# Performance work log

Measured on AMD Instinct MI355X. Metric: run time of the kernel, lower is better.

## Reference

```python
import jax, jax.numpy as jnp
import numpy as np

B, D, H = 16384, 1024, 16
HD = D // H
EPS = 1e-5


def setup_inputs() -> dict:
    key = jax.random.key(0)
    ks = jax.random.split(key, 16)
    w = lambda k, shape: jax.random.normal(k, shape, jnp.float32) * 0.02
    return {
        "img_emb": jax.random.normal(ks[0], (B, D), jnp.float32),
        "txt_emb": jax.random.normal(ks[1], (B, D), jnp.float32),
        "route_choice": jax.random.randint(ks[2], (B,), 0, 3, jnp.int32),
        # gate: Linear(2D -> D) + sigmoid
        "Wg": w(ks[3], (2 * D, D)), "bg": jnp.zeros((D,), jnp.float32),
        # MultiheadAttention in/out projections
        "Wqkv": w(ks[4], (D, 3 * D)), "bqkv": jnp.zeros((3 * D,), jnp.float32),
        "Wo": w(ks[5], (D, D)), "bo": jnp.zeros((D,), jnp.float32),
        # LayerNorm
        "gamma": jnp.ones((D,), jnp.float32), "beta": jnp.zeros((D,), jnp.float32),
        # FFN: Linear(D->4D), GELU, Linear(4D->D)
        "Wf1": w(ks[6], (D, 4 * D)), "bf1": jnp.zeros((4 * D,), jnp.float32),
        "Wf2": w(ks[7], (4 * D, D)), "bf2": jnp.zeros((D,), jnp.float32),
    }


def _layernorm(x, gamma, beta):
    mu = jnp.mean(x, axis=-1, keepdims=True)
    var = jnp.mean(jnp.square(x - mu), axis=-1, keepdims=True)
    return (x - mu) * jax.lax.rsqrt(var + EPS) * gamma + beta


def reference(img_emb, txt_emb, route_choice, Wg, bg, Wqkv, bqkv, Wo, bo,
              gamma, beta, Wf1, bf1, Wf2, bf2):
    # Eval mode: energy_loss = 0, no dropout. Routing choice supplied as int input.
    # Compute the 'full' fusion branch densely, then select per sample.
    ri = jnp.concatenate([img_emb, txt_emb], axis=-1)          # [B, 2D]
    gate = jax.nn.sigmoid(ri @ Wg + bg)                        # [B, D]
    fused = gate * img_emb + (1.0 - gate) * txt_emb            # [B, D]

    x = jnp.stack([img_emb, txt_emb], axis=1)                  # [B, 2, D]
    qkv = x @ Wqkv + bqkv                                      # [B, 2, 3D]
    q, k, v = jnp.split(qkv, 3, axis=-1)
    q = q.reshape(B, 2, H, HD)
    k = k.reshape(B, 2, H, HD)
    v = v.reshape(B, 2, H, HD)
    scores = jnp.einsum("bqhd,bkhd->bhqk", q, k) / np.sqrt(HD) # [B, H, 2, 2]
    attn = jax.nn.softmax(scores, axis=-1)
    ctx = jnp.einsum("bhqk,bkhd->bqhd", attn, v).reshape(B, 2, D)
    attn_out = ctx @ Wo + bo                                   # [B, 2, D]

    fused = fused + attn_out.mean(axis=1)
    fused = _layernorm(fused, gamma, beta)
    full_out = jax.nn.gelu(fused @ Wf1 + bf1, approximate=False) @ Wf2 + bf2

    rc = route_choice[:, None]
    out = jnp.where(rc == 0, img_emb, jnp.where(rc == 1, txt_emb, full_out))
    return out
```

## Files before the change

### kernel.cpp

```cpp
#include <hip/hip_runtime.h>
#include <hip/hip_bf16.h>
#include <math.h>

#define NB 16384
#define DIM 1024
#define CAP 6656

using bf16 = __hip_bfloat16;
typedef __attribute__((ext_vector_type(8))) short short8;
typedef __attribute__((ext_vector_type(4))) short short4v;
typedef __attribute__((ext_vector_type(4))) float float4v;

enum { EPI_QKV = 1, EPI_GELU = 3, EPI_OUT = 4 };

__device__ __forceinline__ void gl_lds16(const void* g, void* l) {
  __builtin_amdgcn_global_load_lds(
      (const __attribute__((address_space(1))) unsigned int*)g,
      (__attribute__((address_space(3))) unsigned int*)l, 16, 0, 0);
}

__device__ __forceinline__ short f2bf(float x) {
  __hip_bfloat16 h = __float2bfloat16(x);
  return *reinterpret_cast<short*>(&h);
}

__global__ __launch_bounds__(256) void transpose_cast(
    const float* __restrict__ in, bf16* __restrict__ out, int K, int N) {
  __shared__ float tile[32][33];
  int n0 = blockIdx.x * 32, k0 = blockIdx.y * 32;
  int tx = threadIdx.x, ty = threadIdx.y;
#pragma unroll
  for (int i = 0; i < 32; i += 8)
    tile[ty + i][tx] = in[(size_t)(k0 + ty + i) * N + n0 + tx];
  __syncthreads();
#pragma unroll
  for (int i = 0; i < 32; i += 8)
    out[(size_t)(n0 + ty + i) * K + k0 + tx] = __float2bfloat16(tile[tx][ty + i]);
}

__global__ void zero_cnt(int* cnt) { if (threadIdx.x == 0) *cnt = 0; }

__global__ __launch_bounds__(256) void index_build(const int* __restrict__ route,
                                                   int* __restrict__ cnt,
                                                   int* __restrict__ idx) {
  int r = blockIdx.x * 256 + threadIdx.x;
  if (r < NB && route[r] == 2) {
    int p = atomicAdd(cnt, 1);
    idx[p] = r;
  }
}

__global__ __launch_bounds__(256) void gather_cast(
    const float* __restrict__ img, const float* __restrict__ txt,
    const int* __restrict__ cnt, const int* __restrict__ idx,
    bf16* __restrict__ xg, bf16* __restrict__ tg) {
  int n = blockIdx.x;
  if (n >= *cnt) return;
  int r = idx[n];
  int c = threadIdx.x * 4;
  float4 vi = *(const float4*)(img + (size_t)r * DIM + c);
  float4 vt = *(const float4*)(txt + (size_t)r * DIM + c);
  short4v pi, pt;
  pi[0] = f2bf(vi.x); pi[1] = f2bf(vi.y); pi[2] = f2bf(vi.z); pi[3] = f2bf(vi.w);
  pt[0] = f2bf(vt.x); pt[1] = f2bf(vt.y); pt[2] = f2bf(vt.z); pt[3] = f2bf(vt.w);
  *(short4v*)(xg + (size_t)n * DIM + c) = pi;
  *(short4v*)(tg + (size_t)n * DIM + c) = pt;
}

template <int EPI>
__global__ __launch_bounds__(256) void gemm_k(
    const bf16* __restrict__ A0, const bf16* __restrict__ Bt,
    const float* __restrict__ bias, void* __restrict__ outp, int ldo,
    const int* __restrict__ cntp, const int* __restrict__ idx, int K) {
  const int cnt = *cntp;
  const int m0 = blockIdx.y * 128;
  if (m0 >= ((cnt + 127) & ~127)) return;
  alignas(16) __shared__ bf16 sA[128 * 32];
  alignas(16) __shared__ bf16 sB[128 * 32];
  const int t = threadIdx.x;
  const int wave = t >> 6, lane = t & 63;
  const int wm = (wave >> 1) * 64, wn = (wave & 1) * 64;
  const int n0 = blockIdx.x * 128;
  const int r16 = lane & 15, quad = lane >> 4;

  float4v acc[4][4] = {};

  for (int k0 = 0; k0 < K; k0 += 32) {
    if (k0) __syncthreads();
#pragma unroll
    for (int j = 0; j < 2; ++j) {
      int c = t + j * 256;
      int row = c >> 2;
      int kk = k0 + (c & 3) * 8;
      gl_lds16(Bt + (size_t)(n0 + row) * K + kk, (void*)(sB + j * 2048 + wave * 512));
      gl_lds16(A0 + (size_t)(m0 + row) * K + kk, (void*)(sA + j * 2048 + wave * 512));
    }
    __syncthreads();
    short8 af[4], bfr[4];
#pragma unroll
    for (int i = 0; i < 4; ++i) {
      af[i] = *(const short8*)(sA + (wm + i * 16 + r16) * 32 + quad * 8);
      bfr[i] = *(const short8*)(sB + (wn + i * 16 + r16) * 32 + quad * 8);
    }
#pragma unroll
    for (int i = 0; i < 4; ++i)
#pragma unroll
      for (int j = 0; j < 4; ++j)
        acc[i][j] =
            __builtin_amdgcn_mfma_f32_16x16x32_bf16(af[i], bfr[j], acc[i][j], 0, 0, 0);
  }

#pragma unroll
  for (int i = 0; i < 4; ++i) {
#pragma unroll
    for (int j = 0; j < 4; ++j) {
      int gcol = n0 + wn + j * 16 + r16;
      float bv = bias[gcol];
#pragma unroll
      for (int r = 0; r < 4; ++r) {
        int grow = m0 + wm + i * 16 + quad * 4 + r;
        float v = acc[i][j][r] + bv;
        if constexpr (EPI == EPI_QKV) {
          ((bf16*)outp)[(size_t)grow * ldo + gcol] = __float2bfloat16(v);
        } else if constexpr (EPI == EPI_GELU) {
          float gl = 0.5f * v * (1.f + erff(v * 0.70710678118654752f));
          ((bf16*)outp)[(size_t)grow * ldo + gcol] = __float2bfloat16(gl);
        } else {
          if (grow < cnt) {
            int orow = idx[grow];
            ((float*)outp)[(size_t)orow * DIM + gcol] = v;
          }
        }
      }
    }
  }
}

__global__ __launch_bounds__(256) void gate_z_kernel(
    const float* __restrict__ img, const float* __restrict__ txt,
    const bf16* __restrict__ xg, const bf16* __restrict__ tg,
    const bf16* __restrict__ WgT, const float* __restrict__ bg,
    const bf16* __restrict__ WoT, const float* __restrict__ bo,
    const bf16* __restrict__ cmean, bf16* __restrict__ z,
    const int* __restrict__ cntp, const int* __restrict__ idx) {
  const int cnt = *cntp;
  const int m0 = blockIdx.y * 128;
  if (m0 >= ((cnt + 127) & ~127)) return;
  alignas(16) __shared__ bf16 sA[128 * 32];
  alignas(16) __shared__ bf16 sB[128 * 32];
  const int t = threadIdx.x;
  const int wave = t >> 6, lane = t & 63;
  const int wm = (wave >> 1) * 64, wn = (wave & 1) * 64;
  const int n0 = blockIdx.x * 128;
  const int r16 = lane & 15, quad = lane >> 4;

  float4v acc[4][4] = {};
  for (int k0 = 0; k0 < 2048; k0 += 32) {
    if (k0) __syncthreads();
#pragma unroll
    for (int j = 0; j < 2; ++j) {
      int c = t + j * 256;
      int row = c >> 2;
      int kk = k0 + (c & 3) * 8;
      gl_lds16(WgT + (size_t)(n0 + row) * 2048 + kk, (void*)(sB + j * 2048 + wave * 512));
      const bf16* ga = (kk < DIM) ? xg + (size_t)(m0 + row) * DIM + kk
                                  : tg + (size_t)(m0 + row) * DIM + (kk - DIM);
      gl_lds16(ga, (void*)(sA + j * 2048 + wave * 512));
    }
    __syncthreads();
    short8 af[4], bfr[4];
#pragma unroll
    for (int i = 0; i < 4; ++i) {
      af[i] = *(const short8*)(sA + (wm + i * 16 + r16) * 32 + quad * 8);
      bfr[i] = *(const short8*)(sB + (wn + i * 16 + r16) * 32 + quad * 8);
    }
#pragma unroll
    for (int i = 0; i < 4; ++i)
#pragma unroll
      for (int j = 0; j < 4; ++j)
        acc[i][j] =
            __builtin_amdgcn_mfma_f32_16x16x32_bf16(af[i], bfr[j], acc[i][j], 0, 0, 0);
  }
  float4v fmix[4][4];
#pragma unroll
  for (int i = 0; i < 4; ++i)
#pragma unroll
    for (int j = 0; j < 4; ++j) {
      int gcol = n0 + wn + j * 16 + r16;
      float bv = bg[gcol];
#pragma unroll
      for (int r = 0; r < 4; ++r) {
        int grow = m0 + wm + i * 16 + quad * 4 + r;
        float fm = 0.f;
        if (grow < cnt) {
          int orow = idx[grow];
          float g = 1.f / (1.f + expf(-(acc[i][j][r] + bv)));
          size_t ii = (size_t)orow * DIM + gcol;
          fm = g * img[ii] + (1.f - g) * txt[ii];
        }
        fmix[i][j][r] = fm;
        acc[i][j][r] = 0.f;
      }
    }
  __syncthreads();
  for (int k0 = 0; k0 < 1024; k0 += 32) {
    if (k0) __syncthreads();
#pragma unroll
    for (int j = 0; j < 2; ++j) {
      int c = t + j * 256;
      int row = c >> 2;
      int kk = k0 + (c & 3) * 8;
      gl_lds16(cmean + (size_t)(m0 + row) * 1024 + kk, (void*)(sA + j * 2048 + wave * 512));
      gl_lds16(WoT + (size_t)(n0 + row) * 1024 + kk, (void*)(sB + j * 2048 + wave * 512));
    }
    __syncthreads();
    short8 af[4], bfr[4];
#pragma unroll
    for (int i = 0; i < 4; ++i) {
      af[i] = *(const short8*)(sA + (wm + i * 16 + r16) * 32 + quad * 8);
      bfr[i] = *(const short8*)(sB + (wn + i * 16 + r16) * 32 + quad * 8);
    }
#pragma unroll
    for (int i = 0; i < 4; ++i)
#pragma unroll
      for (int j = 0; j < 4; ++j)
        acc[i][j] =
            __builtin_amdgcn_mfma_f32_16x16x32_bf16(af[i], bfr[j], acc[i][j], 0, 0, 0);
  }
#pragma unroll
  for (int i = 0; i < 4; ++i)
#pragma unroll
    for (int j = 0; j < 4; ++j) {
      int gcol = n0 + wn + j * 16 + r16;
      float bv = bo[gcol];
#pragma unroll
      for (int r = 0; r < 4; ++r) {
        int grow = m0 + wm + i * 16 + quad * 4 + r;
        z[(size_t)grow * DIM + gcol] =
            __float2bfloat16(fmix[i][j][r] + acc[i][j][r] + bv);
      }
    }
}

__global__ __launch_bounds__(256) void attn_kernel(const bf16* __restrict__ qkv,
                                                   bf16* __restrict__ cmean,
                                                   const int* __restrict__ cntp) {
  const int cnt = *cntp;
  int gw = blockIdx.x * 4 + (threadIdx.x >> 6);
  int lane = threadIdx.x & 63;
  int n = gw >> 4, h = gw & 15;
  if (n >= ((cnt + 127) & ~127)) return;
  const bf16* b0 = qkv + (size_t)n * 3072 + h * 64 + lane;
  const bf16* b1 = b0 + (size_t)CAP * 3072;
  float q0 = __bfloat162float(b0[0]);
  float k0 = __bfloat162float(b0[1024]);
  float v0 = __bfloat162float(b0[2048]);
  float q1 = __bfloat162float(b1[0]);
  float k1 = __bfloat162float(b1[1024]);
  float v1 = __bfloat162float(b1[2048]);
  float s00 = q0 * k0, s01 = q0 * k1, s10 = q1 * k0, s11 = q1 * k1;
#pragma unroll
  for (int d = 32; d > 0; d >>= 1) {
    s00 += __shfl_xor(s00, d);
    s01 += __shfl_xor(s01, d);
    s10 += __shfl_xor(s10, d);
    s11 += __shfl_xor(s11, d);
  }
  const float sc = 0.125f;
  s00 *= sc; s01 *= sc; s10 *= sc; s11 *= sc;
  float m0 = fmaxf(s00, s01), m1 = fmaxf(s10, s11);
  float e00 = expf(s00 - m0), e01 = expf(s01 - m0);
  float e10 = expf(s10 - m1), e11 = expf(s11 - m1);
  float i0 = 1.f / (e00 + e01), i1 = 1.f / (e10 + e11);
  float c0 = (e00 * i0) * v0 + (e01 * i0) * v1;
  float c1 = (e10 * i1) * v0 + (e11 * i1) * v1;
  cmean[(size_t)n * DIM + h * 64 + lane] = __float2bfloat16(0.5f * (c0 + c1));
}

__global__ __launch_bounds__(256) void ln_kernel(bf16* __restrict__ z,
                                                 const float* __restrict__ g,
                                                 const float* __restrict__ be,
                                                 const int* __restrict__ cntp) {
  const int cnt = *cntp;
  int b = blockIdx.x, t = threadIdx.x;
  if (b >= ((cnt + 127) & ~127)) return;
  bf16* zr = z + (size_t)b * DIM;
  float v[4];
  float s = 0.f, s2 = 0.f;
#pragma unroll
  for (int i = 0; i < 4; ++i) {
    float x = __bfloat162float(zr[t + 256 * i]);
    v[i] = x; s += x; s2 += x * x;
  }
#pragma unroll
  for (int d = 32; d > 0; d >>= 1) {
    s += __shfl_xor(s, d);
    s2 += __shfl_xor(s2, d);
  }
  __shared__ float rs[4], rs2[4];
  int w = t >> 6, lane = t & 63;
  if (!lane) { rs[w] = s; rs2[w] = s2; }
  __syncthreads();
  s = rs[0] + rs[1] + rs[2] + rs[3];
  s2 = rs2[0] + rs2[1] + rs2[2] + rs2[3];
  float mu = s * (1.f / 1024.f);
  float var = s2 * (1.f / 1024.f) - mu * mu;
  float r = rsqrtf(var + 1e-5f);
#pragma unroll
  for (int i = 0; i < 4; ++i) {
    int c = t + 256 * i;
    zr[c] = __float2bfloat16((v[i] - mu) * r * g[c] + be[c]);
  }
}

__global__ __launch_bounds__(256) void copy_out(const float* __restrict__ img,
                                                const float* __restrict__ txt,
                                                const int* __restrict__ route,
                                                float* __restrict__ out) {
  int row = blockIdx.x;
  int rc = route[row];
  if (rc == 2) return;
  const float* src = rc == 0 ? img : txt;
  int c = threadIdx.x * 4;
  *(float4*)(out + (size_t)row * DIM + c) = *(const float4*)(src + (size_t)row * DIM + c);
}

extern "C" void kernel_launch(void* const* d_in, const int* in_sizes, int n_in,
                              void* d_out, int out_size, void* d_ws, size_t ws_size,
                              hipStream_t stream) {
  const float* img = (const float*)d_in[0];
  const float* txt = (const float*)d_in[1];
  const int* route = (const int*)d_in[2];
  const float* Wg = (const float*)d_in[3];
  const float* bg = (const float*)d_in[4];
  const float* Wqkv = (const float*)d_in[5];
  const float* bqkv = (const float*)d_in[6];
  const float* Wo = (const float*)d_in[7];
  const float* bo = (const float*)d_in[8];
  const float* gamma = (const float*)d_in[9];
  const float* beta = (const float*)d_in[10];
  const float* Wf1 = (const float*)d_in[11];
  const float* bf1 = (const float*)d_in[12];
  const float* Wf2 = (const float*)d_in[13];
  const float* bf2 = (const float*)d_in[14];

  char* ws = (char*)d_ws;
  size_t off = 0;
  auto alloc = [&](size_t bytes) {
    char* p = ws + off;
    off += (bytes + 255) & ~(size_t)255;
    return p;
  };
  int* cntp = (int*)alloc(256);
  int* idx = (int*)alloc((size_t)NB * 4);
  bf16* WgT = (bf16*)alloc((size_t)1024 * 2048 * 2);
  bf16* WqkvT = (bf16*)alloc((size_t)3072 * 1024 * 2);
  bf16* WoT = (bf16*)alloc((size_t)1024 * 1024 * 2);
  bf16* Wf1T = (bf16*)alloc((size_t)4096 * 1024 * 2);
  bf16* Wf2T = (bf16*)alloc((size_t)1024 * 4096 * 2);
  bf16* xg = (bf16*)alloc((size_t)CAP * 1024 * 2);
  bf16* tg = (bf16*)alloc((size_t)CAP * 1024 * 2);
  bf16* qkvs = (bf16*)alloc((size_t)2 * CAP * 3072 * 2);
  bf16* cmean = (bf16*)alloc((size_t)CAP * 1024 * 2);
  bf16* zb = (bf16*)alloc((size_t)CAP * 1024 * 2);
  bf16* hb = qkvs;

  const int MB = CAP / 128;
  dim3 tblk(32, 8);
  transpose_cast<<<dim3(1024 / 32, 2048 / 32), tblk, 0, stream>>>(Wg, WgT, 2048, 1024);
  transpose_cast<<<dim3(3072 / 32, 1024 / 32), tblk, 0, stream>>>(Wqkv, WqkvT, 1024, 3072);
  transpose_cast<<<dim3(1024 / 32, 1024 / 32), tblk, 0, stream>>>(Wo, WoT, 1024, 1024);
  transpose_cast<<<dim3(4096 / 32, 1024 / 32), tblk, 0, stream>>>(Wf1, Wf1T, 1024, 4096);
  transpose_cast<<<dim3(1024 / 32, 4096 / 32), tblk, 0, stream>>>(Wf2, Wf2T, 4096, 1024);

  zero_cnt<<<1, 64, 0, stream>>>(cntp);
  index_build<<<NB / 256, 256, 0, stream>>>(route, cntp, idx);
  gather_cast<<<CAP, 256, 0, stream>>>(img, txt, cntp, idx, xg, tg);

  gemm_k<EPI_QKV><<<dim3(24, MB), 256, 0, stream>>>(
      xg, WqkvT, bqkv, qkvs, 3072, cntp, idx, 1024);
  gemm_k<EPI_QKV><<<dim3(24, MB), 256, 0, stream>>>(
      tg, WqkvT, bqkv, qkvs + (size_t)CAP * 3072, 3072, cntp, idx, 1024);
  attn_kernel<<<CAP * 4, 256, 0, stream>>>(qkvs, cmean, cntp);
  gate_z_kernel<<<dim3(8, MB), 256, 0, stream>>>(img, txt, xg, tg, WgT, bg, WoT, bo,
                                                 cmean, zb, cntp, idx);
  ln_kernel<<<CAP, 256, 0, stream>>>(zb, gamma, beta, cntp);
  gemm_k<EPI_GELU><<<dim3(32, MB), 256, 0, stream>>>(
      zb, Wf1T, bf1, hb, 4096, cntp, idx, 1024);
  gemm_k<EPI_OUT><<<dim3(8, MB), 256, 0, stream>>>(
      hb, Wf2T, bf2, d_out, 1024, cntp, idx, 4096);
  copy_out<<<NB, 256, 0, stream>>>(img, txt, route, (float*)d_out);
}
```

Measured before the change: 643.5 us.

## Fuse gate GEMM into QKV GEMMs, split-K FFN2, swizzle tiles, merged routed output

The gate linear is split into its image and text halves and appended as extra output columns to each QKV GEMM (N=4096). The separate gate GEMM inside the Wo kernel goes away, and Wo's epilogue reads the two partial gate pre-activations instead. The second FFN GEMM is split over K into two fp32 partial buffers, which are summed with the bias in a route_out kernel that also copies the non-routed rows. This replaces the scattered fp32 writes with coalesced row writes. Block ids are swizzled in groups of 8 N-tiles to improve L2 reuse, at the cost of extra partial-buffer traffic and a few more launches.

```diff
diff --git a/kernel.cpp b/kernel.cpp
--- a/kernel.cpp
+++ b/kernel.cpp
@@ -5,14 +5,13 @@
 #define NB 16384
 #define DIM 1024
 #define CAP 6656
+#define MT 52
 
 using bf16 = __hip_bfloat16;
 typedef __attribute__((ext_vector_type(8))) short short8;
 typedef __attribute__((ext_vector_type(4))) short short4v;
 typedef __attribute__((ext_vector_type(4))) float float4v;
 
-enum { EPI_QKV = 1, EPI_GELU = 3, EPI_OUT = 4 };
-
 __device__ __forceinline__ void gl_lds16(const void* g, void* l) {
   __builtin_amdgcn_global_load_lds(
       (const __attribute__((address_space(1))) unsigned int*)g,
@@ -22,6 +21,16 @@
 __device__ __forceinline__ short f2bf(float x) {
   __hip_bfloat16 h = __float2bfloat16(x);
   return *reinterpret_cast<short*>(&h);
+}
+
+__device__ __forceinline__ void swz(int bid, int nN, int& m0, int& n0) {
+  int x = bid & 7;
+  int r = bid >> 3;
+  int nl = nN >> 3;
+  int nLoc = r % nl;
+  int m = r / nl;
+  n0 = (x + 8 * nLoc) * 128;
+  m0 = m * 128;
 }
 
 __global__ __launch_bounds__(256) void transpose_cast(
@@ -38,15 +47,27 @@
     out[(size_t)(n0 + ty + i) * K + k0 + tx] = __float2bfloat16(tile[tx][ty + i]);
 }
 
+__global__ __launch_bounds__(256) void fill_bias(const float* __restrict__ bqkv,
+                                                 const float* __restrict__ bg,
+                                                 float* __restrict__ biasA,
+                                                 float* __restrict__ biasB) {
+  int i = blockIdx.x * 256 + threadIdx.x;
+  float qv = (i < 3072) ? bqkv[i] : 0.f;
+  biasA[i] = qv;
+  biasB[i] = (i < 3072) ? qv : bg[i - 3072];
+}
+
 __global__ void zero_cnt(int* cnt) { if (threadIdx.x == 0) *cnt = 0; }
 
 __global__ __launch_bounds__(256) void index_build(const int* __restrict__ route,
                                                    int* __restrict__ cnt,
-                                                   int* __restrict__ idx) {
+                                                   int* __restrict__ idx,
+                                                   int* __restrict__ pos) {
   int r = blockIdx.x * 256 + threadIdx.x;
   if (r < NB && route[r] == 2) {
     int p = atomicAdd(cnt, 1);
     idx[p] = r;
+    pos[r] = p;
   }
 }
 
@@ -67,33 +88,32 @@
   *(short4v*)(tg + (size_t)n * DIM + c) = pt;
 }
 
-template <int EPI>
-__global__ __launch_bounds__(256) void gemm_k(
-    const bf16* __restrict__ A0, const bf16* __restrict__ Bt,
-    const float* __restrict__ bias, void* __restrict__ outp, int ldo,
-    const int* __restrict__ cntp, const int* __restrict__ idx, int K) {
-  const int cnt = *cntp;
-  const int m0 = blockIdx.y * 128;
+__global__ __launch_bounds__(256) void gemm_qkvg(
+    const bf16* __restrict__ A0, const bf16* __restrict__ BtQ,
+    const bf16* __restrict__ BtG, const float* __restrict__ bias,
+    bf16* __restrict__ outp, const int* __restrict__ cntp) {
+  const int cnt = *cntp;
+  int m0, n0;
+  swz(blockIdx.x, 32, m0, n0);
   if (m0 >= ((cnt + 127) & ~127)) return;
   alignas(16) __shared__ bf16 sA[128 * 32];
   alignas(16) __shared__ bf16 sB[128 * 32];
   const int t = threadIdx.x;
   const int wave = t >> 6, lane = t & 63;
   const int wm = (wave >> 1) * 64, wn = (wave & 1) * 64;
-  const int n0 = blockIdx.x * 128;
   const int r16 = lane & 15, quad = lane >> 4;
+  const bf16* Bt = (n0 < 3072) ? BtQ + (size_t)n0 * 1024 : BtG + (size_t)(n0 - 3072) * 1024;
 
   float4v acc[4][4] = {};
-
-  for (int k0 = 0; k0 < K; k0 += 32) {
+  for (int k0 = 0; k0 < 1024; k0 += 32) {
     if (k0) __syncthreads();
 #pragma unroll
     for (int j = 0; j < 2; ++j) {
       int c = t + j * 256;
       int row = c >> 2;
       int kk = k0 + (c & 3) * 8;
-      gl_lds16(Bt + (size_t)(n0 + row) * K + kk, (void*)(sB + j * 2048 + wave * 512));
-      gl_lds16(A0 + (size_t)(m0 + row) * K + kk, (void*)(sA + j * 2048 + wave * 512));
+      gl_lds16(Bt + (size_t)row * 1024 + kk, (void*)(sB + j * 2048 + wave * 512));
+      gl_lds16(A0 + (size_t)(m0 + row) * 1024 + kk, (void*)(sA + j * 2048 + wave * 512));
     }
     __syncthreads();
     short8 af[4], bfr[4];
@@ -109,9 +129,8 @@
         acc[i][j] =
             __builtin_amdgcn_mfma_f32_16x16x32_bf16(af[i], bfr[j], acc[i][j], 0, 0, 0);
   }
-
-#pragma unroll
-  for (int i = 0; i < 4; ++i) {
+#pragma unroll
+  for (int i = 0; i < 4; ++i)
 #pragma unroll
     for (int j = 0; j < 4; ++j) {
       int gcol = n0 + wn + j * 16 + r16;
@@ -119,130 +138,13 @@
 #pragma unroll
       for (int r = 0; r < 4; ++r) {
         int grow = m0 + wm + i * 16 + quad * 4 + r;
-        float v = acc[i][j][r] + bv;
-        if constexpr (EPI == EPI_QKV) {
-          ((bf16*)outp)[(size_t)grow * ldo + gcol] = __float2bfloat16(v);
-        } else if constexpr (EPI == EPI_GELU) {
-          float gl = 0.5f * v * (1.f + erff(v * 0.70710678118654752f));
-          ((bf16*)outp)[(size_t)grow * ldo + gcol] = __float2bfloat16(gl);
-        } else {
-          if (grow < cnt) {
-            int orow = idx[grow];
-            ((float*)outp)[(size_t)orow * DIM + gcol] = v;
-          }
-        }
+        outp[(size_t)grow * 4096 + gcol] = __float2bfloat16(acc[i][j][r] + bv);
       }
     }
-  }
-}
-
-__global__ __launch_bounds__(256) void gate_z_kernel(
-    const float* __restrict__ img, const float* __restrict__ txt,
-    const bf16* __restrict__ xg, const bf16* __restrict__ tg,
-    const bf16* __restrict__ WgT, const float* __restrict__ bg,
-    const bf16* __restrict__ WoT, const float* __restrict__ bo,
-    const bf16* __restrict__ cmean, bf16* __restrict__ z,
-    const int* __restrict__ cntp, const int* __restrict__ idx) {
-  const int cnt = *cntp;
-  const int m0 = blockIdx.y * 128;
-  if (m0 >= ((cnt + 127) & ~127)) return;
-  alignas(16) __shared__ bf16 sA[128 * 32];
-  alignas(16) __shared__ bf16 sB[128 * 32];
-  const int t = threadIdx.x;
-  const int wave = t >> 6, lane = t & 63;
-  const int wm = (wave >> 1) * 64, wn = (wave & 1) * 64;
-  const int n0 = blockIdx.x * 128;
-  const int r16 = lane & 15, quad = lane >> 4;
-
-  float4v acc[4][4] = {};
-  for (int k0 = 0; k0 < 2048; k0 += 32) {
-    if (k0) __syncthreads();
-#pragma unroll
-    for (int j = 0; j < 2; ++j) {
-      int c = t + j * 256;
-      int row = c >> 2;
-      int kk = k0 + (c & 3) * 8;
-      gl_lds16(WgT + (size_t)(n0 + row) * 2048 + kk, (void*)(sB + j * 2048 + wave * 512));
-      const bf16* ga = (kk < DIM) ? xg + (size_t)(m0 + row) * DIM + kk
-                                  : tg + (size_t)(m0 + row) * DIM + (kk - DIM);
-      gl_lds16(ga, (void*)(sA + j * 2048 + wave * 512));
-    }
-    __syncthreads();
-    short8 af[4], bfr[4];
-#pragma unroll
-    for (int i = 0; i < 4; ++i) {
-      af[i] = *(const short8*)(sA + (wm + i * 16 + r16) * 32 + quad * 8);
-      bfr[i] = *(const short8*)(sB + (wn + i * 16 + r16) * 32 + quad * 8);
-    }
-#pragma unroll
-    for (int i = 0; i < 4; ++i)
-#pragma unroll
-      for (int j = 0; j < 4; ++j)
-        acc[i][j] =
-            __builtin_amdgcn_mfma_f32_16x16x32_bf16(af[i], bfr[j], acc[i][j], 0, 0, 0);
-  }
-  float4v fmix[4][4];
-#pragma unroll
-  for (int i = 0; i < 4; ++i)
-#pragma unroll
-    for (int j = 0; j < 4; ++j) {
-      int gcol = n0 + wn + j * 16 + r16;
-      float bv = bg[gcol];
-#pragma unroll
-      for (int r = 0; r < 4; ++r) {
-        int grow = m0 + wm + i * 16 + quad * 4 + r;
-        float fm = 0.f;
-        if (grow < cnt) {
-          int orow = idx[grow];
-          float g = 1.f / (1.f + expf(-(acc[i][j][r] + bv)));
-          size_t ii = (size_t)orow * DIM + gcol;
-          fm = g * img[ii] + (1.f - g) * txt[ii];
-        }
-        fmix[i][j][r] = fm;
-        acc[i][j][r] = 0.f;
-      }
-    }
-  __syncthreads();
-  for (int k0 = 0; k0 < 1024; k0 += 32) {
-    if (k0) __syncthreads();
-#pragma unroll
-    for (int j = 0; j < 2; ++j) {
-      int c = t + j * 256;
-      int row = c >> 2;
-      int kk = k0 + (c & 3) * 8;
-      gl_lds16(cmean + (size_t)(m0 + row) * 1024 + kk, (void*)(sA + j * 2048 + wave * 512));
-      gl_lds16(WoT + (size_t)(n0 + row) * 1024 + kk, (void*)(sB + j * 2048 + wave * 512));
-    }
-    __syncthreads();
-    short8 af[4], bfr[4];
-#pragma unroll
-    for (int i = 0; i < 4; ++i) {
-      af[i] = *(const short8*)(sA + (wm + i * 16 + r16) * 32 + quad * 8);
-      bfr[i] = *(const short8*)(sB + (wn + i * 16 + r16) * 32 + quad * 8);
-    }
-#pragma unroll
-    for (int i = 0; i < 4; ++i)
-#pragma unroll
-      for (int j = 0; j < 4; ++j)
-        acc[i][j] =
-            __builtin_amdgcn_mfma_f32_16x16x32_bf16(af[i], bfr[j], acc[i][j], 0, 0, 0);
-  }
-#pragma unroll
-  for (int i = 0; i < 4; ++i)
-#pragma unroll
-    for (int j = 0; j < 4; ++j) {
-      int gcol = n0 + wn + j * 16 + r16;
-      float bv = bo[gcol];
-#pragma unroll
-      for (int r = 0; r < 4; ++r) {
-        int grow = m0 + wm + i * 16 + quad * 4 + r;
-        z[(size_t)grow * DIM + gcol] =
-            __float2bfloat16(fmix[i][j][r] + acc[i][j][r] + bv);
-      }
-    }
-}
-
-__global__ __launch_bounds__(256) void attn_kernel(const bf16* __restrict__ qkv,
+}
+
+__global__ __launch_bounds__(256) void attn_kernel(const bf16* __restrict__ qx,
+                                                   const bf16* __restrict__ tx,
                                                    bf16* __restrict__ cmean,
                                                    const int* __restrict__ cntp) {
   const int cnt = *cntp;
@@ -250,8 +152,8 @@
   int lane = threadIdx.x & 63;
   int n = gw >> 4, h = gw & 15;
   if (n >= ((cnt + 127) & ~127)) return;
-  const bf16* b0 = qkv + (size_t)n * 3072 + h * 64 + lane;
-  const bf16* b1 = b0 + (size_t)CAP * 3072;
+  const bf16* b0 = qx + (size_t)n * 4096 + h * 64 + lane;
+  const bf16* b1 = tx + (size_t)n * 4096 + h * 64 + lane;
   float q0 = __bfloat162float(b0[0]);
   float k0 = __bfloat162float(b0[1024]);
   float v0 = __bfloat162float(b0[2048]);
@@ -277,6 +179,72 @@
   cmean[(size_t)n * DIM + h * 64 + lane] = __float2bfloat16(0.5f * (c0 + c1));
 }
 
+__global__ __launch_bounds__(256) void wo_z_kernel(
+    const float* __restrict__ img, const float* __restrict__ txt,
+    const bf16* __restrict__ qx, const bf16* __restrict__ tx,
+    const bf16* __restrict__ WoT, const float* __restrict__ bg,
+    const float* __restrict__ bo, const bf16* __restrict__ cmean,
+    bf16* __restrict__ z, const int* __restrict__ cntp, const int* __restrict__ idx) {
+  const int cnt = *cntp;
+  int m0, n0;
+  swz(blockIdx.x, 8, m0, n0);
+  if (m0 >= ((cnt + 127) & ~127)) return;
+  alignas(16) __shared__ bf16 sA[128 * 32];
+  alignas(16) __shared__ bf16 sB[128 * 32];
+  const int t = threadIdx.x;
+  const int wave = t >> 6, lane = t & 63;
+  const int wm = (wave >> 1) * 64, wn = (wave & 1) * 64;
+  const int r16 = lane & 15, quad = lane >> 4;
+
+  float4v acc[4][4] = {};
+  for (int k0 = 0; k0 < 1024; k0 += 32) {
+    if (k0) __syncthreads();
+#pragma unroll
+    for (int j = 0; j < 2; ++j) {
+      int c = t + j * 256;
+      int row = c >> 2;
+      int kk = k0 + (c & 3) * 8;
+      gl_lds16(WoT + (size_t)(n0 + row) * 1024 + kk, (void*)(sB + j * 2048 + wave * 512));
+      gl_lds16(cmean + (size_t)(m0 + row) * 1024 + kk, (void*)(sA + j * 2048 + wave * 512));
+    }
+    __syncthreads();
+    short8 af[4], bfr[4];
+#pragma unroll
+    for (int i = 0; i < 4; ++i) {
+      af[i] = *(const short8*)(sA + (wm + i * 16 + r16) * 32 + quad * 8);
+      bfr[i] = *(const short8*)(sB + (wn + i * 16 + r16) * 32 + quad * 8);
+    }
+#pragma unroll
+    for (int i = 0; i < 4; ++i)
+#pragma unroll
+      for (int j = 0; j < 4; ++j)
+        acc[i][j] =
+            __builtin_amdgcn_mfma_f32_16x16x32_bf16(af[i], bfr[j], acc[i][j], 0, 0, 0);
+  }
+#pragma unroll
+  for (int i = 0; i < 4; ++i)
+#pragma unroll
+    for (int j = 0; j < 4; ++j) {
+      int gcol = n0 + wn + j * 16 + r16;
+      float bgv = bg[gcol], bov = bo[gcol];
+#pragma unroll
+      for (int r = 0; r < 4; ++r) {
+        int grow = m0 + wm + i * 16 + quad * 4 + r;
+        float zv = 0.f;
+        if (grow < cnt) {
+          int orow = idx[grow];
+          float gp = __bfloat162float(qx[(size_t)grow * 4096 + 3072 + gcol]) +
+                     __bfloat162float(tx[(size_t)grow * 4096 + 3072 + gcol]) + bgv;
+          float g = 1.f / (1.f + expf(-gp));
+          size_t ii = (size_t)orow * DIM + gcol;
+          float fm = g * img[ii] + (1.f - g) * txt[ii];
+          zv = fm + acc[i][j][r] + bov;
+        }
+        z[(size_t)grow * DIM + gcol] = __float2bfloat16(zv);
+      }
+    }
+}
+
 __global__ __launch_bounds__(256) void ln_kernel(bf16* __restrict__ z,
                                                  const float* __restrict__ g,
                                                  const float* __restrict__ be,
@@ -313,16 +281,142 @@
   }
 }
 
-__global__ __launch_bounds__(256) void copy_out(const float* __restrict__ img,
-                                                const float* __restrict__ txt,
-                                                const int* __restrict__ route,
-                                                float* __restrict__ out) {
+__global__ __launch_bounds__(256) void gemm_gelu(
+    const bf16* __restrict__ A0, const bf16* __restrict__ Bt,
+    const float* __restrict__ bias, bf16* __restrict__ outp,
+    const int* __restrict__ cntp) {
+  const int cnt = *cntp;
+  int m0, n0;
+  swz(blockIdx.x, 32, m0, n0);
+  if (m0 >= ((cnt + 127) & ~127)) return;
+  alignas(16) __shared__ bf16 sA[128 * 32];
+  alignas(16) __shared__ bf16 sB[128 * 32];
+  const int t = threadIdx.x;
+  const int wave = t >> 6, lane = t & 63;
+  const int wm = (wave >> 1) * 64, wn = (wave & 1) * 64;
+  const int r16 = lane & 15, quad = lane >> 4;
+
+  float4v acc[4][4] = {};
+  for (int k0 = 0; k0 < 1024; k0 += 32) {
+    if (k0) __syncthreads();
+#pragma unroll
+    for (int j = 0; j < 2; ++j) {
+      int c = t + j * 256;
+      int row = c >> 2;
+      int kk = k0 + (c & 3) * 8;
+      gl_lds16(Bt + (size_t)(n0 + row) * 1024 + kk, (void*)(sB + j * 2048 + wave * 512));
+      gl_lds16(A0 + (size_t)(m0 + row) * 1024 + kk, (void*)(sA + j * 2048 + wave * 512));
+    }
+    __syncthreads();
+    short8 af[4], bfr[4];
+#pragma unroll
+    for (int i = 0; i < 4; ++i) {
+      af[i] = *(const short8*)(sA + (wm + i * 16 + r16) * 32 + quad * 8);
+      bfr[i] = *(const short8*)(sB + (wn + i * 16 + r16) * 32 + quad * 8);
+    }
+#pragma unroll
+    for (int i = 0; i < 4; ++i)
+#pragma unroll
+      for (int j = 0; j < 4; ++j)
+        acc[i][j] =
+            __builtin_amdgcn_mfma_f32_16x16x32_bf16(af[i], bfr[j], acc[i][j], 0, 0, 0);
+  }
+#pragma unroll
+  for (int i = 0; i < 4; ++i)
+#pragma unroll
+    for (int j = 0; j < 4; ++j) {
+      int gcol = n0 + wn + j * 16 + r16;
+      float bv = bias[gcol];
+#pragma unroll
+      for (int r = 0; r < 4; ++r) {
+        int grow = m0 + wm + i * 16 + quad * 4 + r;
+        float v = acc[i][j][r] + bv;
+        float gl = 0.5f * v * (1.f + erff(v * 0.70710678118654752f));
+        outp[(size_t)grow * 4096 + gcol] = __float2bfloat16(gl);
+      }
+    }
+}
+
+__global__ __launch_bounds__(256) void gemm_splitk(
+    const bf16* __restrict__ A0, const bf16* __restrict__ Bt,
+    float* __restrict__ parts, const int* __restrict__ cntp) {
+  const int cnt = *cntp;
+  const int nblk = 8 * MT;
+  int s = blockIdx.x / nblk;
+  int bid = blockIdx.x % nblk;
+  int m0, n0;
+  swz(bid, 8, m0, n0);
+  if (m0 >= ((cnt + 127) & ~127)) return;
+  alignas(16) __shared__ bf16 sA[128 * 32];
+  alignas(16) __shared__ bf16 sB[128 * 32];
+  const int t = threadIdx.x;
+  const int wave = t >> 6, lane = t & 63;
+  const int wm = (wave >> 1) * 64, wn = (wave & 1) * 64;
+  const int r16 = lane & 15, quad = lane >> 4;
+  const int kbase = s * 2048;
+
+  float4v acc[4][4] = {};
+  for (int k0 = kbase; k0 < kbase + 2048; k0 += 32) {
+    if (k0 != kbase) __syncthreads();
+#pragma unroll
+    for (int j = 0; j < 2; ++j) {
+      int c = t + j * 256;
+      int row = c >> 2;
+      int kk = k0 + (c & 3) * 8;
+      gl_lds16(Bt + (size_t)(n0 + row) * 4096 + kk, (void*)(sB + j * 2048 + wave * 512));
+      gl_lds16(A0 + (size_t)(m0 + row) * 4096 + kk, (void*)(sA + j * 2048 + wave * 512));
+    }
+    __syncthreads();
+    short8 af[4], bfr[4];
+#pragma unroll
+    for (int i = 0; i < 4; ++i) {
+      af[i] = *(const short8*)(sA + (wm + i * 16 + r16) * 32 + quad * 8);
+      bfr[i] = *(const short8*)(sB + (wn + i * 16 + r16) * 32 + quad * 8);
+    }
+#pragma unroll
+    for (int i = 0; i < 4; ++i)
+#pragma unroll
+      for (int j = 0; j < 4; ++j)
+        acc[i][j] =
+            __builtin_amdgcn_mfma_f32_16x16x32_bf16(af[i], bfr[j], acc[i][j], 0, 0, 0);
+  }
+  float* out = parts + (size_t)s * CAP * 1024;
+#pragma unroll
+  for (int i = 0; i < 4; ++i)
+#pragma unroll
+    for (int j = 0; j < 4; ++j) {
+      int gcol = n0 + wn + j * 16 + r16;
+#pragma unroll
+      for (int r = 0; r < 4; ++r) {
+        int grow = m0 + wm + i * 16 + quad * 4 + r;
+        out[(size_t)grow * 1024 + gcol] = acc[i][j][r];
+      }
+    }
+}
+
+__global__ __launch_bounds__(256) void route_out(
+    const float* __restrict__ img, const float* __restrict__ txt,
+    const int* __restrict__ route, const int* __restrict__ pos,
+    const float* __restrict__ parts, const float* __restrict__ bf2,
+    float* __restrict__ out) {
   int row = blockIdx.x;
   int rc = route[row];
-  if (rc == 2) return;
-  const float* src = rc == 0 ? img : txt;
   int c = threadIdx.x * 4;
-  *(float4*)(out + (size_t)row * DIM + c) = *(const float4*)(src + (size_t)row * DIM + c);
+  float4 v;
+  if (rc == 2) {
+    int n = pos[row];
+    float4 p0 = *(const float4*)(parts + (size_t)n * 1024 + c);
+    float4 p1 = *(const float4*)(parts + (size_t)CAP * 1024 + (size_t)n * 1024 + c);
+    float4 b = *(const float4*)(bf2 + c);
+    v.x = p0.x + p1.x + b.x;
+    v.y = p0.y + p1.y + b.y;
+    v.z = p0.z + p1.z + b.z;
+    v.w = p0.w + p1.w + b.w;
+  } else {
+    const float* src = (rc == 0) ? img : txt;
+    v = *(const float4*)(src + (size_t)row * DIM + c);
+  }
+  *(float4*)(out + (size_t)row * DIM + c) = v;
 }
 
 extern "C" void kernel_launch(void* const* d_in, const int* in_sizes, int n_in,
@@ -353,41 +447,44 @@
   };
   int* cntp = (int*)alloc(256);
   int* idx = (int*)alloc((size_t)NB * 4);
-  bf16* WgT = (bf16*)alloc((size_t)1024 * 2048 * 2);
+  int* pos = (int*)alloc((size_t)NB * 4);
+  float* biasA = (float*)alloc(4096 * 4);
+  float* biasB = (float*)alloc(4096 * 4);
   bf16* WqkvT = (bf16*)alloc((size_t)3072 * 1024 * 2);
+  bf16* WgTopT = (bf16*)alloc((size_t)1024 * 1024 * 2);
+  bf16* WgBotT = (bf16*)alloc((size_t)1024 * 1024 * 2);
   bf16* WoT = (bf16*)alloc((size_t)1024 * 1024 * 2);
   bf16* Wf1T = (bf16*)alloc((size_t)4096 * 1024 * 2);
   bf16* Wf2T = (bf16*)alloc((size_t)1024 * 4096 * 2);
   bf16* xg = (bf16*)alloc((size_t)CAP * 1024 * 2);
   bf16* tg = (bf16*)alloc((size_t)CAP * 1024 * 2);
-  bf16* qkvs = (bf16*)alloc((size_t)2 * CAP * 3072 * 2);
+  bf16* qx = (bf16*)alloc((size_t)CAP * 4096 * 2);
+  bf16* tx = (bf16*)alloc((size_t)CAP * 4096 * 2);
   bf16* cmean = (bf16*)alloc((size_t)CAP * 1024 * 2);
   bf16* zb = (bf16*)alloc((size_t)CAP * 1024 * 2);
-  bf16* hb = qkvs;
-
-  const int MB = CAP / 128;
+  bf16* hb = qx;
+  float* parts = (float*)tx;
+
   dim3 tblk(32, 8);
-  transpose_cast<<<dim3(1024 / 32, 2048 / 32), tblk, 0, stream>>>(Wg, WgT, 2048, 1024);
   transpose_cast<<<dim3(3072 / 32, 1024 / 32), tblk, 0, stream>>>(Wqkv, WqkvT, 1024, 3072);
+  transpose_cast<<<dim3(1024 / 32, 1024 / 32), tblk, 0, stream>>>(Wg, WgTopT, 1024, 1024);
+  transpose_cast<<<dim3(1024 / 32, 1024 / 32), tblk, 0, stream>>>(Wg + 1024 * 1024, WgBotT, 1024, 1024);
   transpose_cast<<<dim3(1024 / 32, 1024 / 32), tblk, 0, stream>>>(Wo, WoT, 1024, 1024);
   transpose_cast<<<dim3(4096 / 32, 1024 / 32), tblk, 0, stream>>>(Wf1, Wf1T, 1024, 4096);
   transpose_cast<<<dim3(1024 / 32, 4096 / 32), tblk, 0, stream>>>(Wf2, Wf2T, 4096, 1024);
+  fill_bias<<<16, 256, 0, stream>>>(bqkv, bg, biasA, biasB);
 
   zero_cnt<<<1, 64, 0, stream>>>(cntp);
-  index_build<<<NB / 256, 256, 0, stream>>>(route, cntp, idx);
+  index_build<<<NB / 256, 256, 0, stream>>>(route, cntp, idx, pos);
   gather_cast<<<CAP, 256, 0, stream>>>(img, txt, cntp, idx, xg, tg);
 
-  gemm_k<EPI_QKV><<<dim3(24, MB), 256, 0, stream>>>(
-      xg, WqkvT, bqkv, qkvs, 3072, cntp, idx, 1024);
-  gemm_k<EPI_QKV><<<dim3(24, MB), 256, 0, stream>>>(
-      tg, WqkvT, bqkv, qkvs + (size_t)CAP * 3072, 3072, cntp, idx, 1024);
-  attn_kernel<<<CAP * 4, 256, 0, stream>>>(qkvs, cmean, cntp);
-  gate_z_kernel<<<dim3(8, MB), 256, 0, stream>>>(img, txt, xg, tg, WgT, bg, WoT, bo,
-                                                 cmean, zb, cntp, idx);
+  gemm_qkvg<<<32 * MT, 256, 0, stream>>>(xg, WqkvT, WgTopT, biasA, qx, cntp);
+  gemm_qkvg<<<32 * MT, 256, 0, stream>>>(tg, WqkvT, WgBotT, biasB, tx, cntp);
+  attn_kernel<<<CAP * 4, 256, 0, stream>>>(qx, tx, cmean, cntp);
+  wo_z_kernel<<<8 * MT, 256, 0, stream>>>(img, txt, qx, tx, WoT, bg, bo, cmean, zb,
+                                          cntp, idx);
   ln_kernel<<<CAP, 256, 0, stream>>>(zb, gamma, beta, cntp);
-  gemm_k<EPI_GELU><<<dim3(32, MB), 256, 0, stream>>>(
-      zb, Wf1T, bf1, hb, 4096, cntp, idx, 1024);
-  gemm_k<EPI_OUT><<<dim3(8, MB), 256, 0, stream>>>(
-      hb, Wf2T, bf2, d_out, 1024, cntp, idx, 4096);
-  copy_out<<<NB, 256, 0, stream>>>(img, txt, route, (float*)d_out);
-}
+  gemm_gelu<<<32 * MT, 256, 0, stream>>>(zb, Wf1T, bf1, hb, cntp);
+  gemm_splitk<<<2 * 8 * MT, 256, 0, stream>>>(hb, Wf2T, parts, cntp);
+  route_out<<<NB, 256, 0, stream>>>(img, txt, route, pos, parts, bf2, (float*)d_out);
+}
```

Result: faster. 595.7 us (-7.4%).
